# Optimization experiments

Hardware: AMD Instinct MI355X
Metric: run time of the kernel (lower is better)

## Reference

```python
import jax, jax.numpy as jnp
import numpy as np

F = 64  # dim_features
DIM_TASK = 32


def setup_inputs() -> dict:
    key = jax.random.key(0)
    ks = jax.random.split(key, 16)
    n_state, n_task, n_actor = 65536, 32768, 32768
    E_st, E_ta = 2_000_000, 1_000_000
    inp = {
        'x_state': jax.random.normal(ks[0], (n_state, F), jnp.float32),
        'x_task': jax.random.normal(ks[1], (n_task, F), jnp.float32),
        'x_actor': jax.random.normal(ks[2], (n_actor, F), jnp.float32),
        'edge_attr': jax.random.normal(ks[3], (E_st, 2), jnp.float32),
        # GINEConv edge linear: Linear(2 -> F)
        'We': jax.random.normal(ks[4], (2, F), jnp.float32) * 0.5,
        'be': jnp.zeros((F,), jnp.float32),
        # GinStandardMLP: Linear(F,F) -> ReLU -> Linear(F,F)
        'W1a': jax.random.normal(ks[5], (F, F), jnp.float32) / np.sqrt(F),
        'b1a': jnp.zeros((F,), jnp.float32),
        'W1b': jax.random.normal(ks[6], (F, F), jnp.float32) / np.sqrt(F),
        'b1b': jnp.zeros((F,), jnp.float32),
        # UnactivatedMLP: Linear(F,F) -> ReLU -> Linear(F,1)
        'W2a': jax.random.normal(ks[7], (F, F), jnp.float32) / np.sqrt(F),
        'b2a': jnp.zeros((F,), jnp.float32),
        'W2b': jax.random.normal(ks[8], (F, 1), jnp.float32) / np.sqrt(F),
        'b2b': jnp.zeros((1,), jnp.float32),
        'src_st': jax.random.randint(ks[9], (E_st,), 0, n_state, jnp.int32),
        'dst_st': jax.random.randint(ks[10], (E_st,), 0, n_task, jnp.int32),
        'src_ta': jax.random.randint(ks[11], (E_ta,), 0, n_task, jnp.int32),
        'dst_ta': jax.random.randint(ks[12], (E_ta,), 0, n_actor, jnp.int32),
    }
    return inp


def reference(x_state, x_task, x_actor, edge_attr, We, be, W1a, b1a, W1b, b1b,
              W2a, b2a, W2b, b2b, src_st, dst_st, src_ta, dst_ta):
    n_task = x_task.shape[0]
    n_actor = x_actor.shape[0]
    # --- GINEConv (eps=0): agg_i = sum_e relu(x_src[e] + lin(edge_attr[e])) ---
    msg = jax.nn.relu(x_state[src_st] + edge_attr @ We + be)  # [E_st, F]
    agg = jax.ops.segment_sum(msg, dst_st, num_segments=n_task)  # [n_task, F]
    h = x_task + agg  # (1+eps)*x_r + agg, eps=0
    # GinStandardMLP: Linear-ReLU-Linear
    x1 = jax.nn.relu(h @ W1a + b1a) @ W1b + b1b  # [n_task, F]
    # --- GINConv (eps=0): agg2_i = sum_e x1[src[e]] ---
    agg2 = jax.ops.segment_sum(x1[src_ta], dst_ta, num_segments=n_actor)  # [n_actor, F]
    h2 = x_actor + agg2
    # UnactivatedMLP: Linear-ReLU-Linear -> 1
    logits = jax.nn.relu(h2 @ W2a + b2a) @ W2b + b2b  # [n_actor, 1]
    return logits.reshape(-1, DIM_TASK)
```

## Files before the change

kernel.cpp:

```cpp
#include <hip/hip_runtime.h>

#define F 64
#define TILE 4096
#define NB 1024
#define ROWSB 32
#define CAP1 2560
#define CAP2 1408

typedef __attribute__((ext_vector_type(8))) short bf8;
typedef __attribute__((ext_vector_type(4))) float f4;
typedef __attribute__((ext_vector_type(2))) float fl2;

__device__ __forceinline__ unsigned short f2bf(float f) {
    unsigned u = __float_as_uint(f);
    unsigned r = u + 0x7fffu + ((u >> 16) & 1u);
    return (unsigned short)(r >> 16);
}
__device__ __forceinline__ float bf2f(unsigned short h) {
    return __uint_as_float((unsigned)h << 16);
}
__device__ __forceinline__ fl2 unpack2(unsigned d) {
    fl2 r;
    r.x = __uint_as_float(d << 16);
    r.y = __uint_as_float(d & 0xffff0000u);
    return r;
}

__global__ __launch_bounds__(1024) void prep_kernel(
    const float4* __restrict__ xs4, ushort4* __restrict__ xsb4, int n4,
    const int* __restrict__ src1, const int* __restrict__ dst1,
    const float* __restrict__ ea, int E1,
    int* __restrict__ cur1, uint2* __restrict__ keyA1,
    const int* __restrict__ src2, const int* __restrict__ dst2, int E2,
    int* __restrict__ cur2, unsigned* __restrict__ keyA2,
    int nCvt, int nBin1)
{
    __shared__ uint2 stage[TILE];
    __shared__ int hist[NB], scanb[NB], lstart[NB], lcur[NB], gbase[NB];
    int bid = blockIdx.x;
    int tid = threadIdx.x;

    if (bid < nCvt) {
        int i = bid * 1024 + tid;
        if (i < n4) {
            float4 v = xs4[i];
            ushort4 o;
            o.x = f2bf(v.x); o.y = f2bf(v.y); o.z = f2bf(v.z); o.w = f2bf(v.w);
            xsb4[i] = o;
        }
        return;
    }

    if (bid < nCvt + nBin1) {
        int base = (bid - nCvt) * TILE;
        int cnt = min(TILE, E1 - base);
        hist[tid] = 0;
        __syncthreads();
        int myb[4];
        #pragma unroll
        for (int j = 0; j < 4; ++j) {
            int idx = tid + 1024 * j;
            if (idx < cnt) {
                int b = dst1[base + idx] >> 5;
                myb[j] = b;
                atomicAdd(&hist[b], 1);
            } else myb[j] = -1;
        }
        __syncthreads();
        int c = hist[tid];
        gbase[tid] = CAP1 * tid + atomicAdd(&cur1[tid], c);
        scanb[tid] = c;
        __syncthreads();
        for (int off = 1; off < NB; off <<= 1) {
            int u = (tid >= off) ? scanb[tid - off] : 0;
            __syncthreads();
            scanb[tid] += u;
            __syncthreads();
        }
        int excl = scanb[tid] - c;
        lstart[tid] = excl;
        lcur[tid] = excl;
        __syncthreads();
        #pragma unroll
        for (int j = 0; j < 4; ++j) {
            int idx = tid + 1024 * j;
            if (idx < cnt) {
                int b = myb[j];
                int p = atomicAdd(&lcur[b], 1);
                float2 e2 = ((const float2* __restrict__)ea)[base + idx];
                unsigned sd = ((unsigned)src1[base + idx] << 16) | (unsigned)dst1[base + idx];
                unsigned pk = ((unsigned)f2bf(e2.y) << 16) | (unsigned)f2bf(e2.x);
                stage[p] = make_uint2(sd, pk);
            }
        }
        __syncthreads();
        #pragma unroll
        for (int j = 0; j < 4; ++j) {
            int p = tid + 1024 * j;
            if (p < cnt) {
                uint2 f = stage[p];
                int b = (int)(f.x & 0xffffu) >> 5;
                keyA1[gbase[b] + (p - lstart[b])] = f;
            }
        }
        return;
    }

    {
        unsigned* ustage = (unsigned*)stage;
        int base = (bid - nCvt - nBin1) * TILE;
        int cnt = min(TILE, E2 - base);
        hist[tid] = 0;
        __syncthreads();
        int myb[4];
        #pragma unroll
        for (int j = 0; j < 4; ++j) {
            int idx = tid + 1024 * j;
            if (idx < cnt) {
                int b = dst2[base + idx] >> 5;
                myb[j] = b;
                atomicAdd(&hist[b], 1);
            } else myb[j] = -1;
        }
        __syncthreads();
        int c = hist[tid];
        gbase[tid] = CAP2 * tid + atomicAdd(&cur2[tid], c);
        scanb[tid] = c;
        __syncthreads();
        for (int off = 1; off < NB; off <<= 1) {
            int u = (tid >= off) ? scanb[tid - off] : 0;
            __syncthreads();
            scanb[tid] += u;
            __syncthreads();
        }
        int excl = scanb[tid] - c;
        lstart[tid] = excl;
        lcur[tid] = excl;
        __syncthreads();
        #pragma unroll
        for (int j = 0; j < 4; ++j) {
            int idx = tid + 1024 * j;
            if (idx < cnt) {
                int b = myb[j];
                int p = atomicAdd(&lcur[b], 1);
                ustage[p] = ((unsigned)src2[base + idx] << 16) | (unsigned)dst2[base + idx];
            }
        }
        __syncthreads();
        #pragma unroll
        for (int j = 0; j < 4; ++j) {
            int p = tid + 1024 * j;
            if (p < cnt) {
                unsigned f = ustage[p];
                int b = (int)(f & 0xffffu) >> 5;
                keyA2[gbase[b] + (p - lstart[b])] = f;
            }
        }
    }
}

__global__ __launch_bounds__(512) void sg1_kernel(
    const uint2* __restrict__ keyA,
    const ushort* __restrict__ xsb,
    const float* __restrict__ x_task,
    const float* __restrict__ We, const float* __restrict__ be,
    const int* __restrict__ gcursor,
    float* __restrict__ hout, int n)
{
    __shared__ uint2 lpay[CAP1];
    __shared__ int hh[ROWSB], rst[ROWSB], cur[ROWSB];
    __shared__ float hbuf[8][F + 4];
    int tid = threadIdx.x;
    int b = blockIdx.x;
    int cnt = min(gcursor[b], CAP1);
    const uint2* ka = keyA + (size_t)b * CAP1;

    if (tid < ROWSB) hh[tid] = 0;
    __syncthreads();

    uint2 myk[5];
    #pragma unroll
    for (int j = 0; j < 5; ++j) {
        int idx = tid + 512 * j;
        if (idx < cnt) {
            myk[j] = ka[idx];
            atomicAdd(&hh[myk[j].x & 31u], 1);
        }
    }
    __syncthreads();
    if (tid < ROWSB) cur[tid] = hh[tid];
    __syncthreads();
    for (int off = 1; off < ROWSB; off <<= 1) {
        int u = (tid < ROWSB && tid >= off) ? cur[tid - off] : 0;
        __syncthreads();
        if (tid < ROWSB) cur[tid] += u;
        __syncthreads();
    }
    if (tid < ROWSB) {
        int excl = cur[tid] - hh[tid];
        rst[tid] = excl;
        cur[tid] = excl;
    }
    __syncthreads();
    #pragma unroll
    for (int j = 0; j < 5; ++j) {
        int idx = tid + 512 * j;
        if (idx < cnt) {
            int p = atomicAdd(&cur[myk[j].x & 31u], 1);
            lpay[p] = myk[j];
        }
    }
    __syncthreads();

    int wave = tid >> 6, lane = tid & 63;
    int q = lane & 7, g = lane >> 3;
    fl2 w0p[4], w1p[4], bbp[4];
    {
        float4 a0 = ((const float4* __restrict__)We)[q * 2];
        float4 a1 = ((const float4* __restrict__)We)[q * 2 + 1];
        float4 c0 = ((const float4* __restrict__)(We + F))[q * 2];
        float4 c1 = ((const float4* __restrict__)(We + F))[q * 2 + 1];
        float4 d0 = ((const float4* __restrict__)be)[q * 2];
        float4 d1 = ((const float4* __restrict__)be)[q * 2 + 1];
        w0p[0] = (fl2){a0.x, a0.y}; w0p[1] = (fl2){a0.z, a0.w};
        w0p[2] = (fl2){a1.x, a1.y}; w0p[3] = (fl2){a1.z, a1.w};
        w1p[0] = (fl2){c0.x, c0.y}; w1p[1] = (fl2){c0.z, c0.w};
        w1p[2] = (fl2){c1.x, c1.y}; w1p[3] = (fl2){c1.z, c1.w};
        bbp[0] = (fl2){d0.x, d0.y}; bbp[1] = (fl2){d0.z, d0.w};
        bbp[2] = (fl2){d1.x, d1.y}; bbp[3] = (fl2){d1.z, d1.w};
    }
    const fl2 zero2 = {0.f, 0.f};

    for (int r = wave; r < ROWSB; r += 8) {
        int row = b * ROWSB + r;
        if (row >= n) break;
        int start = rst[r];
        int c = hh[r];
        fl2 acc2[4];
        #pragma unroll
        for (int p = 0; p < 4; ++p) acc2[p] = zero2;

        #define SG1_BODY(ii)                                                     \
        {                                                                        \
            uint2 pe = lpay[start + (ii)];                                       \
            int s = (int)(pe.x >> 16);                                           \
            fl2 ex = {__uint_as_float(pe.y << 16), __uint_as_float(pe.y << 16)}; \
            fl2 ey = {__uint_as_float(pe.y & 0xffff0000u),                       \
                      __uint_as_float(pe.y & 0xffff0000u)};                      \
            uint4 xw = ((const uint4* __restrict__)(xsb + (size_t)s * F))[q];    \
            fl2 cc, t;                                                           \
            cc = __builtin_elementwise_fma(ey, w1p[0], bbp[0]);                  \
            cc = __builtin_elementwise_fma(ex, w0p[0], cc);                      \
            t = unpack2(xw.x) + cc;                                              \
            acc2[0] += __builtin_elementwise_max(t, zero2);                      \
            cc = __builtin_elementwise_fma(ey, w1p[1], bbp[1]);                  \
            cc = __builtin_elementwise_fma(ex, w0p[1], cc);                      \
            t = unpack2(xw.y) + cc;                                              \
            acc2[1] += __builtin_elementwise_max(t, zero2);                      \
            cc = __builtin_elementwise_fma(ey, w1p[2], bbp[2]);                  \
            cc = __builtin_elementwise_fma(ex, w0p[2], cc);                      \
            t = unpack2(xw.z) + cc;                                              \
            acc2[2] += __builtin_elementwise_max(t, zero2);                      \
            cc = __builtin_elementwise_fma(ey, w1p[3], bbp[3]);                  \
            cc = __builtin_elementwise_fma(ex, w0p[3], cc);                      \
            t = unpack2(xw.w) + cc;                                              \
            acc2[3] += __builtin_elementwise_max(t, zero2);                      \
        }

        int i = g;
        for (; i + 8 < c; i += 16) { SG1_BODY(i); SG1_BODY(i + 8); }
        for (; i < c; i += 8) SG1_BODY(i);
        #undef SG1_BODY

        float acc[8];
        #pragma unroll
        for (int p = 0; p < 4; ++p) { acc[2 * p] = acc2[p].x; acc[2 * p + 1] = acc2[p].y; }
        #pragma unroll
        for (int j = 0; j < 8; ++j) {
            acc[j] += __shfl_xor(acc[j], 8);
            acc[j] += __shfl_xor(acc[j], 16);
            acc[j] += __shfl_xor(acc[j], 32);
        }
        if (g == 0) {
            #pragma unroll
            for (int j = 0; j < 8; ++j)
                hbuf[wave][q * 8 + j] = acc[j];
        }
        float h = hbuf[wave][lane] + x_task[(size_t)row * F + lane];
        hout[(size_t)row * F + lane] = h;
    }
}

__global__ __launch_bounds__(256) void mlp1_kernel(
    const float* __restrict__ hin,
    const float* __restrict__ W1a, const float* __restrict__ b1a,
    const float* __restrict__ W1b, const float* __restrict__ b1b,
    ushort* __restrict__ x1b, int n)
{
    __shared__ float ldsH[4][16 * 68];
    int tid = threadIdx.x;
    int wave = tid >> 6, lane = tid & 63;
    int quad = lane >> 4, col = lane & 15;
    int rowbase = blockIdx.x * 64 + wave * 16;
    if (rowbase >= n) return;
    float* ltile = ldsH[wave];

    bf8 Wah[2][4], Wal[2][4], Wbh[2][4], Wbl[2][4];
    float ba1[4], bb1[4];
    #pragma unroll
    for (int kh = 0; kh < 2; ++kh)
        #pragma unroll
        for (int c = 0; c < 4; ++c) {
            bf8 th, tl, sh, sl;
            #pragma unroll
            for (int j = 0; j < 8; ++j) {
                int k = kh * 32 + quad * 8 + j;
                float wa = W1a[k * F + c * 16 + col];
                unsigned short h1 = f2bf(wa);
                th[j] = (short)h1; tl[j] = (short)f2bf(wa - bf2f(h1));
                float wb = W1b[k * F + c * 16 + col];
                unsigned short h2 = f2bf(wb);
                sh[j] = (short)h2; sl[j] = (short)f2bf(wb - bf2f(h2));
            }
            Wah[kh][c] = th; Wal[kh][c] = tl;
            Wbh[kh][c] = sh; Wbl[kh][c] = sl;
        }
    #pragma unroll
    for (int c = 0; c < 4; ++c) { ba1[c] = b1a[c * 16 + col]; bb1[c] = b1b[c * 16 + col]; }

    const float* hrow = hin + (size_t)(rowbase + col) * F + quad * 8;
    bf8 Ah[2], Al[2];
    #pragma unroll
    for (int kh = 0; kh < 2; ++kh) {
        bf8 th, tl;
        #pragma unroll
        for (int j = 0; j < 8; ++j) {
            float a = hrow[kh * 32 + j];
            unsigned short h1 = f2bf(a);
            th[j] = (short)h1; tl[j] = (short)f2bf(a - bf2f(h1));
        }
        Ah[kh] = th; Al[kh] = tl;
    }

    #pragma unroll
    for (int c = 0; c < 4; ++c) {
        f4 acc = {0.f, 0.f, 0.f, 0.f};
        #pragma unroll
        for (int kh = 0; kh < 2; ++kh) {
            acc = __builtin_amdgcn_mfma_f32_16x16x32_bf16(Ah[kh], Wah[kh][c], acc, 0, 0, 0);
            acc = __builtin_amdgcn_mfma_f32_16x16x32_bf16(Ah[kh], Wal[kh][c], acc, 0, 0, 0);
            acc = __builtin_amdgcn_mfma_f32_16x16x32_bf16(Al[kh], Wah[kh][c], acc, 0, 0, 0);
        }
        #pragma unroll
        for (int r = 0; r < 4; ++r)
            ltile[(quad * 4 + r) * 68 + c * 16 + col] = fmaxf(acc[r] + ba1[c], 0.f);
    }
    bf8 A2h[2], A2l[2];
    #pragma unroll
    for (int kh = 0; kh < 2; ++kh) {
        bf8 th, tl;
        #pragma unroll
        for (int j = 0; j < 8; ++j) {
            float a = ltile[col * 68 + kh * 32 + quad * 8 + j];
            unsigned short h1 = f2bf(a);
            th[j] = (short)h1; tl[j] = (short)f2bf(a - bf2f(h1));
        }
        A2h[kh] = th; A2l[kh] = tl;
    }
    #pragma unroll
    for (int c = 0; c < 4; ++c) {
        f4 acc = {0.f, 0.f, 0.f, 0.f};
        #pragma unroll
        for (int kh = 0; kh < 2; ++kh) {
            acc = __builtin_amdgcn_mfma_f32_16x16x32_bf16(A2h[kh], Wbh[kh][c], acc, 0, 0, 0);
            acc = __builtin_amdgcn_mfma_f32_16x16x32_bf16(A2h[kh], Wbl[kh][c], acc, 0, 0, 0);
            acc = __builtin_amdgcn_mfma_f32_16x16x32_bf16(A2l[kh], Wbh[kh][c], acc, 0, 0, 0);
        }
        #pragma unroll
        for (int r = 0; r < 4; ++r)
            ltile[(quad * 4 + r) * 68 + c * 16 + col] = acc[r] + bb1[c];
    }
    int rr = lane >> 2, cc = (lane & 3) * 16;
    unsigned o[8];
    #pragma unroll
    for (int j = 0; j < 8; ++j) {
        unsigned lo = f2bf(ltile[rr * 68 + cc + 2 * j]);
        unsigned hi = f2bf(ltile[rr * 68 + cc + 2 * j + 1]);
        o[j] = lo | (hi << 16);
    }
    uint4* dst = (uint4*)(x1b + (size_t)(rowbase + rr) * F + cc);
    dst[0] = make_uint4(o[0], o[1], o[2], o[3]);
    dst[1] = make_uint4(o[4], o[5], o[6], o[7]);
}

__global__ __launch_bounds__(512) void sg2_kernel(
    const unsigned* __restrict__ keyA,
    const ushort* __restrict__ x1b,
    const float* __restrict__ x_actor,
    const int* __restrict__ gcursor,
    float* __restrict__ h2out, int n)
{
    __shared__ unsigned lpay[CAP2];
    __shared__ int hh[ROWSB], rst[ROWSB], cur[ROWSB];
    __shared__ float hbuf[8][F + 4];
    int tid = threadIdx.x;
    int b = blockIdx.x;
    int cnt = min(gcursor[b], CAP2);
    const unsigned* ka = keyA + (size_t)b * CAP2;

    if (tid < ROWSB) hh[tid] = 0;
    __syncthreads();

    unsigned myk[3];
    #pragma unroll
    for (int j = 0; j < 3; ++j) {
        int idx = tid + 512 * j;
        if (idx < cnt) {
            myk[j] = ka[idx];
            atomicAdd(&hh[myk[j] & 31u], 1);
        }
    }
    __syncthreads();
    if (tid < ROWSB) cur[tid] = hh[tid];
    __syncthreads();
    for (int off = 1; off < ROWSB; off <<= 1) {
        int u = (tid < ROWSB && tid >= off) ? cur[tid - off] : 0;
        __syncthreads();
        if (tid < ROWSB) cur[tid] += u;
        __syncthreads();
    }
    if (tid < ROWSB) {
        int excl = cur[tid] - hh[tid];
        rst[tid] = excl;
        cur[tid] = excl;
    }
    __syncthreads();
    #pragma unroll
    for (int j = 0; j < 3; ++j) {
        int idx = tid + 512 * j;
        if (idx < cnt) {
            int p = atomicAdd(&cur[myk[j] & 31u], 1);
            lpay[p] = myk[j];
        }
    }
    __syncthreads();

    int wave = tid >> 6, lane = tid & 63;
    int q = lane & 7, g = lane >> 3;
    const fl2 zero2 = {0.f, 0.f};
    for (int r = wave; r < ROWSB; r += 8) {
        int row = b * ROWSB + r;
        if (row >= n) break;
        int start = rst[r];
        int c = hh[r];
        fl2 acc2[4];
        #pragma unroll
        for (int p = 0; p < 4; ++p) acc2[p] = zero2;

        #define SG2_BODY(ii)                                                  \
        {                                                                     \
            unsigned sd = lpay[start + (ii)];                                 \
            int s = (int)(sd >> 16);                                          \
            uint4 xw = ((const uint4* __restrict__)(x1b + (size_t)s * F))[q]; \
            acc2[0] += unpack2(xw.x);                                         \
            acc2[1] += unpack2(xw.y);                                         \
            acc2[2] += unpack2(xw.z);                                         \
            acc2[3] += unpack2(xw.w);                                         \
        }

        int i = g;
        for (; i + 8 < c; i += 16) { SG2_BODY(i); SG2_BODY(i + 8); }
        for (; i < c; i += 8) SG2_BODY(i);
        #undef SG2_BODY

        float acc[8];
        #pragma unroll
        for (int p = 0; p < 4; ++p) { acc[2 * p] = acc2[p].x; acc[2 * p + 1] = acc2[p].y; }
        #pragma unroll
        for (int j = 0; j < 8; ++j) {
            acc[j] += __shfl_xor(acc[j], 8);
            acc[j] += __shfl_xor(acc[j], 16);
            acc[j] += __shfl_xor(acc[j], 32);
        }
        if (g == 0) {
            #pragma unroll
            for (int j = 0; j < 8; ++j)
                hbuf[wave][q * 8 + j] = acc[j];
        }
        float h = hbuf[wave][lane] + x_actor[(size_t)row * F + lane];
        h2out[(size_t)row * F + lane] = h;
    }
}

__global__ __launch_bounds__(256) void mlp2_kernel(
    const float* __restrict__ h2in,
    const float* __restrict__ W2a, const float* __restrict__ b2a,
    const float* __restrict__ W2b, const float* __restrict__ b2b,
    float* __restrict__ out, int n)
{
    int tid = threadIdx.x;
    int wave = tid >> 6, lane = tid & 63;
    int quad = lane >> 4, col = lane & 15;
    int rowbase = blockIdx.x * 64 + wave * 16;
    if (rowbase >= n) return;

    bf8 Wah[2][4], Wal[2][4];
    float ba1[4], wo[4];
    #pragma unroll
    for (int kh = 0; kh < 2; ++kh)
        #pragma unroll
        for (int c = 0; c < 4; ++c) {
            bf8 th, tl;
            #pragma unroll
            for (int j = 0; j < 8; ++j) {
                int k = kh * 32 + quad * 8 + j;
                float w = W2a[k * F + c * 16 + col];
                unsigned short h1 = f2bf(w);
                th[j] = (short)h1; tl[j] = (short)f2bf(w - bf2f(h1));
            }
            Wah[kh][c] = th; Wal[kh][c] = tl;
        }
    #pragma unroll
    for (int c = 0; c < 4; ++c) { ba1[c] = b2a[c * 16 + col]; wo[c] = W2b[c * 16 + col]; }
    float bias2 = b2b[0];

    const float* hrow = h2in + (size_t)(rowbase + col) * F + quad * 8;
    bf8 Ah[2], Al[2];
    #pragma unroll
    for (int kh = 0; kh < 2; ++kh) {
        bf8 th, tl;
        #pragma unroll
        for (int j = 0; j < 8; ++j) {
            float a = hrow[kh * 32 + j];
            unsigned short h1 = f2bf(a);
            th[j] = (short)h1; tl[j] = (short)f2bf(a - bf2f(h1));
        }
        Ah[kh] = th; Al[kh] = tl;
    }

    float partial[4] = {0.f, 0.f, 0.f, 0.f};
    #pragma unroll
    for (int c = 0; c < 4; ++c) {
        f4 acc = {0.f, 0.f, 0.f, 0.f};
        #pragma unroll
        for (int kh = 0; kh < 2; ++kh) {
            acc = __builtin_amdgcn_mfma_f32_16x16x32_bf16(Ah[kh], Wah[kh][c], acc, 0, 0, 0);
            acc = __builtin_amdgcn_mfma_f32_16x16x32_bf16(Ah[kh], Wal[kh][c], acc, 0, 0, 0);
            acc = __builtin_amdgcn_mfma_f32_16x16x32_bf16(Al[kh], Wah[kh][c], acc, 0, 0, 0);
        }
        #pragma unroll
        for (int r = 0; r < 4; ++r)
            partial[r] += fmaxf(acc[r] + ba1[c], 0.f) * wo[c];
    }
    #pragma unroll
    for (int off = 1; off < 16; off <<= 1)
        #pragma unroll
        for (int r = 0; r < 4; ++r)
            partial[r] += __shfl_xor(partial[r], off);
    if (col == 0) {
        #pragma unroll
        for (int r = 0; r < 4; ++r)
            out[rowbase + quad * 4 + r] = partial[r] + bias2;
    }
}

extern "C" void kernel_launch(void* const* d_in, const int* in_sizes, int n_in,
                              void* d_out, int out_size, void* d_ws, size_t ws_size,
                              hipStream_t stream)
{
    const float* x_state   = (const float*)d_in[0];
    const float* x_task    = (const float*)d_in[1];
    const float* x_actor   = (const float*)d_in[2];
    const float* edge_attr = (const float*)d_in[3];
    const float* We        = (const float*)d_in[4];
    const float* be        = (const float*)d_in[5];
    const float* W1a       = (const float*)d_in[6];
    const float* b1a       = (const float*)d_in[7];
    const float* W1b       = (const float*)d_in[8];
    const float* b1b       = (const float*)d_in[9];
    const float* W2a       = (const float*)d_in[10];
    const float* b2a       = (const float*)d_in[11];
    const float* W2b       = (const float*)d_in[12];
    const float* b2b       = (const float*)d_in[13];
    const int*   src_st    = (const int*)d_in[14];
    const int*   dst_st    = (const int*)d_in[15];
    const int*   src_ta    = (const int*)d_in[16];
    const int*   dst_ta    = (const int*)d_in[17];

    int n_state = in_sizes[0] / F;
    int n_task  = in_sizes[1] / F;
    int n_actor = in_sizes[2] / F;
    int E_st    = in_sizes[14];
    int E_ta    = in_sizes[16];

    ushort*   x1b   = (ushort*)d_ws;
    float*    hbig  = (float*)(x1b + (size_t)n_task * F);
    ushort*   xsb   = (ushort*)(hbig + (size_t)n_task * F);
    uint2*    keyA1 = (uint2*)(xsb + (size_t)n_state * F);
    unsigned* keyA2 = (unsigned*)(keyA1 + (size_t)NB * CAP1);
    int*      cur1  = (int*)(keyA2 + (size_t)NB * CAP2);
    int*      cur2  = cur1 + NB;

    int n4    = n_state * F / 4;
    int nCvt  = (n4 + 1023) / 1024;
    int nBin1 = (E_st + TILE - 1) / TILE;
    int nBin2 = (E_ta + TILE - 1) / TILE;

    hipMemsetAsync(cur1, 0, 2 * NB * sizeof(int), stream);
    prep_kernel<<<nCvt + nBin1 + nBin2, 1024, 0, stream>>>(
        (const float4*)x_state, (ushort4*)xsb, n4,
        src_st, dst_st, edge_attr, E_st, cur1, keyA1,
        src_ta, dst_ta, E_ta, cur2, keyA2,
        nCvt, nBin1);
    sg1_kernel<<<NB, 512, 0, stream>>>(
        keyA1, xsb, x_task, We, be, cur1, hbig, n_task);
    mlp1_kernel<<<(n_task + 63) / 64, 256, 0, stream>>>(
        hbig, W1a, b1a, W1b, b1b, x1b, n_task);
    sg2_kernel<<<NB, 512, 0, stream>>>(
        keyA2, x1b, x_actor, cur2, hbig, n_actor);
    mlp2_kernel<<<(n_actor + 63) / 64, 256, 0, stream>>>(
        hbig, W2a, b2a, W2b, b2b, (float*)d_out, n_actor);
}
```

Measured before the change: 232.1 us.

## Assign half-row per lane group with software-pipelined gathers in segment-sum kernels

Both segment-sum kernels change the work split. Before, each wave looped over rows and its 8 lane groups strided over the edges. Now each 8-lane group owns half of one row's edge list, with the two halves combined by a single shuffle and the result written straight from registers with float4 stores. The edge loop is software-pipelined with four gathered loads in flight, to hide gather latency and to remove the LDS reduction buffer and the cross-group shuffles. The trade-off is more live registers and possible load imbalance when a row has many edges.

```diff
diff --git a/kernel.cpp b/kernel.cpp
--- a/kernel.cpp
+++ b/kernel.cpp
@@ -169,7 +169,6 @@
 {
     __shared__ uint2 lpay[CAP1];
     __shared__ int hh[ROWSB], rst[ROWSB], cur[ROWSB];
-    __shared__ float hbuf[8][F + 4];
     int tid = threadIdx.x;
     int b = blockIdx.x;
     int cnt = min(gcursor[b], CAP1);
@@ -214,6 +213,11 @@
 
     int wave = tid >> 6, lane = tid & 63;
     int q = lane & 7, g = lane >> 3;
+    int gid = (wave << 3) | g;
+    int r   = gid >> 1;
+    int h   = gid & 1;
+    int row = b * ROWSB + r;
+
     fl2 w0p[4], w1p[4], bbp[4];
     {
         float4 a0 = ((const float4* __restrict__)We)[q * 2];
@@ -231,63 +235,80 @@
     }
     const fl2 zero2 = {0.f, 0.f};
 
-    for (int r = wave; r < ROWSB; r += 8) {
-        int row = b * ROWSB + r;
-        if (row >= n) break;
-        int start = rst[r];
-        int c = hh[r];
-        fl2 acc2[4];
-        #pragma unroll
-        for (int p = 0; p < 4; ++p) acc2[p] = zero2;
-
-        #define SG1_BODY(ii)                                                     \
-        {                                                                        \
-            uint2 pe = lpay[start + (ii)];                                       \
-            int s = (int)(pe.x >> 16);                                           \
-            fl2 ex = {__uint_as_float(pe.y << 16), __uint_as_float(pe.y << 16)}; \
-            fl2 ey = {__uint_as_float(pe.y & 0xffff0000u),                       \
-                      __uint_as_float(pe.y & 0xffff0000u)};                      \
-            uint4 xw = ((const uint4* __restrict__)(xsb + (size_t)s * F))[q];    \
-            fl2 cc, t;                                                           \
-            cc = __builtin_elementwise_fma(ey, w1p[0], bbp[0]);                  \
-            cc = __builtin_elementwise_fma(ex, w0p[0], cc);                      \
-            t = unpack2(xw.x) + cc;                                              \
-            acc2[0] += __builtin_elementwise_max(t, zero2);                      \
-            cc = __builtin_elementwise_fma(ey, w1p[1], bbp[1]);                  \
-            cc = __builtin_elementwise_fma(ex, w0p[1], cc);                      \
-            t = unpack2(xw.y) + cc;                                              \
-            acc2[1] += __builtin_elementwise_max(t, zero2);                      \
-            cc = __builtin_elementwise_fma(ey, w1p[2], bbp[2]);                  \
-            cc = __builtin_elementwise_fma(ex, w0p[2], cc);                      \
-            t = unpack2(xw.z) + cc;                                              \
-            acc2[2] += __builtin_elementwise_max(t, zero2);                      \
-            cc = __builtin_elementwise_fma(ey, w1p[3], bbp[3]);                  \
-            cc = __builtin_elementwise_fma(ex, w0p[3], cc);                      \
-            t = unpack2(xw.w) + cc;                                              \
-            acc2[3] += __builtin_elementwise_max(t, zero2);                      \
-        }
-
-        int i = g;
-        for (; i + 8 < c; i += 16) { SG1_BODY(i); SG1_BODY(i + 8); }
-        for (; i < c; i += 8) SG1_BODY(i);
-        #undef SG1_BODY
-
-        float acc[8];
-        #pragma unroll
-        for (int p = 0; p < 4; ++p) { acc[2 * p] = acc2[p].x; acc[2 * p + 1] = acc2[p].y; }
-        #pragma unroll
-        for (int j = 0; j < 8; ++j) {
-            acc[j] += __shfl_xor(acc[j], 8);
-            acc[j] += __shfl_xor(acc[j], 16);
-            acc[j] += __shfl_xor(acc[j], 32);
-        }
-        if (g == 0) {
-            #pragma unroll
-            for (int j = 0; j < 8; ++j)
-                hbuf[wave][q * 8 + j] = acc[j];
-        }
-        float h = hbuf[wave][lane] + x_task[(size_t)row * F + lane];
-        hout[(size_t)row * F + lane] = h;
+    int c  = hh[r];
+    int m0 = (c + 1) >> 1;
+    int sh = rst[r] + (h ? m0 : 0);
+    int m  = h ? (c - m0) : m0;
+
+    fl2 acc2[4];
+    #pragma unroll
+    for (int p = 0; p < 4; ++p) acc2[p] = zero2;
+
+    unsigned pk0 = 0, pk1 = 0, pk2 = 0, pk3 = 0;
+    uint4 xw0 = {0,0,0,0}, xw1 = {0,0,0,0}, xw2 = {0,0,0,0}, xw3 = {0,0,0,0};
+
+    #define SG1_LOAD(J, K)                                                          \
+    if ((K) < m) {                                                                  \
+        uint2 t = lpay[sh + (K)];                                                   \
+        pk##J = t.y;                                                                \
+        xw##J = ((const uint4* __restrict__)(xsb + ((size_t)(t.x >> 16) << 6)))[q]; \
+    }
+
+    #define SG1_COMP(PK, XW)                                                        \
+    {                                                                               \
+        fl2 ex = {__uint_as_float((PK) << 16), __uint_as_float((PK) << 16)};        \
+        fl2 ey = {__uint_as_float((PK) & 0xffff0000u),                              \
+                  __uint_as_float((PK) & 0xffff0000u)};                             \
+        fl2 cc, t2;                                                                 \
+        cc = __builtin_elementwise_fma(ey, w1p[0], bbp[0]);                         \
+        cc = __builtin_elementwise_fma(ex, w0p[0], cc);                             \
+        t2 = unpack2((XW).x) + cc;                                                  \
+        acc2[0] += __builtin_elementwise_max(t2, zero2);                            \
+        cc = __builtin_elementwise_fma(ey, w1p[1], bbp[1]);                         \
+        cc = __builtin_elementwise_fma(ex, w0p[1], cc);                             \
+        t2 = unpack2((XW).y) + cc;                                                  \
+        acc2[1] += __builtin_elementwise_max(t2, zero2);                            \
+        cc = __builtin_elementwise_fma(ey, w1p[2], bbp[2]);                         \
+        cc = __builtin_elementwise_fma(ex, w0p[2], cc);                             \
+        t2 = unpack2((XW).z) + cc;                                                  \
+        acc2[2] += __builtin_elementwise_max(t2, zero2);                            \
+        cc = __builtin_elementwise_fma(ey, w1p[3], bbp[3]);                         \
+        cc = __builtin_elementwise_fma(ex, w0p[3], cc);                             \
+        t2 = unpack2((XW).w) + cc;                                                  \
+        acc2[3] += __builtin_elementwise_max(t2, zero2);                            \
+    }
+
+    SG1_LOAD(0, 0)
+    SG1_LOAD(1, 1)
+    SG1_LOAD(2, 2)
+    SG1_LOAD(3, 3)
+    int i = 0;
+    for (; i + 4 <= m; i += 4) {
+        SG1_COMP(pk0, xw0) SG1_LOAD(0, i + 4)
+        SG1_COMP(pk1, xw1) SG1_LOAD(1, i + 5)
+        SG1_COMP(pk2, xw2) SG1_LOAD(2, i + 6)
+        SG1_COMP(pk3, xw3) SG1_LOAD(3, i + 7)
+    }
+    if (i < m)     SG1_COMP(pk0, xw0)
+    if (i + 1 < m) SG1_COMP(pk1, xw1)
+    if (i + 2 < m) SG1_COMP(pk2, xw2)
+    #undef SG1_LOAD
+    #undef SG1_COMP
+
+    float acc[8];
+    #pragma unroll
+    for (int p = 0; p < 4; ++p) { acc[2 * p] = acc2[p].x; acc[2 * p + 1] = acc2[p].y; }
+    #pragma unroll
+    for (int j = 0; j < 8; ++j) acc[j] += __shfl_xor(acc[j], 8);
+
+    if (h == 0 && row < n) {
+        const float4* xt = (const float4* __restrict__)(x_task + (size_t)row * F + q * 8);
+        float4 t0 = xt[0], t1 = xt[1];
+        float4 o0, o1;
+        o0.x = acc[0] + t0.x; o0.y = acc[1] + t0.y; o0.z = acc[2] + t0.z; o0.w = acc[3] + t0.w;
+        o1.x = acc[4] + t1.x; o1.y = acc[5] + t1.y; o1.z = acc[6] + t1.z; o1.w = acc[7] + t1.w;
+        float4* hp = (float4*)(hout + (size_t)row * F + q * 8);
+        hp[0] = o0; hp[1] = o1;
     }
 }
 
@@ -402,7 +423,6 @@
 {
     __shared__ unsigned lpay[CAP2];
     __shared__ int hh[ROWSB], rst[ROWSB], cur[ROWSB];
-    __shared__ float hbuf[8][F + 4];
     int tid = threadIdx.x;
     int b = blockIdx.x;
     int cnt = min(gcursor[b], CAP2);
@@ -447,48 +467,68 @@
 
     int wave = tid >> 6, lane = tid & 63;
     int q = lane & 7, g = lane >> 3;
+    int gid = (wave << 3) | g;
+    int r   = gid >> 1;
+    int h   = gid & 1;
+    int row = b * ROWSB + r;
     const fl2 zero2 = {0.f, 0.f};
-    for (int r = wave; r < ROWSB; r += 8) {
-        int row = b * ROWSB + r;
-        if (row >= n) break;
-        int start = rst[r];
-        int c = hh[r];
-        fl2 acc2[4];
-        #pragma unroll
-        for (int p = 0; p < 4; ++p) acc2[p] = zero2;
-
-        #define SG2_BODY(ii)                                                  \
-        {                                                                     \
-            unsigned sd = lpay[start + (ii)];                                 \
-            int s = (int)(sd >> 16);                                          \
-            uint4 xw = ((const uint4* __restrict__)(x1b + (size_t)s * F))[q]; \
-            acc2[0] += unpack2(xw.x);                                         \
-            acc2[1] += unpack2(xw.y);                                         \
-            acc2[2] += unpack2(xw.z);                                         \
-            acc2[3] += unpack2(xw.w);                                         \
-        }
-
-        int i = g;
-        for (; i + 8 < c; i += 16) { SG2_BODY(i); SG2_BODY(i + 8); }
-        for (; i < c; i += 8) SG2_BODY(i);
-        #undef SG2_BODY
-
-        float acc[8];
-        #pragma unroll
-        for (int p = 0; p < 4; ++p) { acc[2 * p] = acc2[p].x; acc[2 * p + 1] = acc2[p].y; }
-        #pragma unroll
-        for (int j = 0; j < 8; ++j) {
-            acc[j] += __shfl_xor(acc[j], 8);
-            acc[j] += __shfl_xor(acc[j], 16);
-            acc[j] += __shfl_xor(acc[j], 32);
-        }
-        if (g == 0) {
-            #pragma unroll
-            for (int j = 0; j < 8; ++j)
-                hbuf[wave][q * 8 + j] = acc[j];
-        }
-        float h = hbuf[wave][lane] + x_actor[(size_t)row * F + lane];
-        h2out[(size_t)row * F + lane] = h;
+
+    int c  = hh[r];
+    int m0 = (c + 1) >> 1;
+    int sh = rst[r] + (h ? m0 : 0);
+    int m  = h ? (c - m0) : m0;
+
+    fl2 acc2[4];
+    #pragma unroll
+    for (int p = 0; p < 4; ++p) acc2[p] = zero2;
+
+    uint4 xw0 = {0,0,0,0}, xw1 = {0,0,0,0}, xw2 = {0,0,0,0}, xw3 = {0,0,0,0};
+
+    #define SG2_LOAD(J, K)                                                          \
+    if ((K) < m) {                                                                  \
+        unsigned t = lpay[sh + (K)];                                                \
+        xw##J = ((const uint4* __restrict__)(x1b + ((size_t)(t >> 16) << 6)))[q];   \
+    }
+
+    #define SG2_COMP(XW)                                                            \
+    {                                                                               \
+        acc2[0] += unpack2((XW).x);                                                 \
+        acc2[1] += unpack2((XW).y);                                                 \
+        acc2[2] += unpack2((XW).z);                                                 \
+        acc2[3] += unpack2((XW).w);                                                 \
+    }
+
+    SG2_LOAD(0, 0)
+    SG2_LOAD(1, 1)
+    SG2_LOAD(2, 2)
+    SG2_LOAD(3, 3)
+    int i = 0;
+    for (; i + 4 <= m; i += 4) {
+        SG2_COMP(xw0) SG2_LOAD(0, i + 4)
+        SG2_COMP(xw1) SG2_LOAD(1, i + 5)
+        SG2_COMP(xw2) SG2_LOAD(2, i + 6)
+        SG2_COMP(xw3) SG2_LOAD(3, i + 7)
+    }
+    if (i < m)     SG2_COMP(xw0)
+    if (i + 1 < m) SG2_COMP(xw1)
+    if (i + 2 < m) SG2_COMP(xw2)
+    #undef SG2_LOAD
+    #undef SG2_COMP
+
+    float acc[8];
+    #pragma unroll
+    for (int p = 0; p < 4; ++p) { acc[2 * p] = acc2[p].x; acc[2 * p + 1] = acc2[p].y; }
+    #pragma unroll
+    for (int j = 0; j < 8; ++j) acc[j] += __shfl_xor(acc[j], 8);
+
+    if (h == 0 && row < n) {
+        const float4* xt = (const float4* __restrict__)(x_actor + (size_t)row * F + q * 8);
+        float4 t0 = xt[0], t1 = xt[1];
+        float4 o0, o1;
+        o0.x = acc[0] + t0.x; o0.y = acc[1] + t0.y; o0.z = acc[2] + t0.z; o0.w = acc[3] + t0.w;
+        o1.x = acc[4] + t1.x; o1.y = acc[5] + t1.y; o1.z = acc[6] + t1.z; o1.w = acc[7] + t1.w;
+        float4* hp = (float4*)(h2out + (size_t)row * F + q * 8);
+        hp[0] = o0; hp[1] = o1;
     }
 }
 
```

New measurement: 224.8 us. -3.1%, faster.
